# Optimization experiments

Measured on AMD Instinct MI355X. Metric: run time of the kernel, lower is better.

Reference implementation:

```python
import jax, jax.numpy as jnp
import numpy as np

B, V, E = 8, 12288, 147456
C_FM, C_U, C_IN, C_HID, C_OUT = 384, 61, 64, 128, 32
EPS = 0.005


def grid_sample_bilinear(img, grid):
    """torch.F.grid_sample, mode='bilinear', padding='zeros', align_corners=False.
    img: (B,C,H,W); grid: (B,Hg,Wg,2) in [-1,1] (x,y). Returns (B,C,Hg,Wg)."""
    Bn, C, H, W = img.shape
    x = (grid[..., 0] + 1.0) * 0.5 * W - 0.5
    y = (grid[..., 1] + 1.0) * 0.5 * H - 0.5
    x0 = jnp.floor(x); y0 = jnp.floor(y)
    wx1 = x - x0; wy1 = y - y0
    wx0 = 1.0 - wx1; wy0 = 1.0 - wy1
    x0i = x0.astype(jnp.int32); y0i = y0.astype(jnp.int32)

    def gather(iy, ix):
        valid = (ix >= 0) & (ix < W) & (iy >= 0) & (iy < H)
        ixc = jnp.clip(ix, 0, W - 1)
        iyc = jnp.clip(iy, 0, H - 1)
        v = jax.vmap(lambda im, yy, xx: im[:, yy, xx])(img, iyc, ixc)  # (B,C,Hg,Wg)
        return v * valid[:, None].astype(img.dtype)

    out = (gather(y0i, x0i) * (wy0 * wx0)[:, None]
           + gather(y0i, x0i + 1) * (wy0 * wx1)[:, None]
           + gather(y0i + 1, x0i) * (wy1 * wx0)[:, None]
           + gather(y0i + 1, x0i + 1) * (wy1 * wx1)[:, None])
    return out


def setup_inputs() -> dict:
    key = jax.random.key(0)
    ks = jax.random.split(key, 12)
    vertices = jax.random.normal(ks[0], (B, V, 3), jnp.float32) * 0.3
    fz = jnp.full((B,), 0.005, jnp.float32) + jax.random.uniform(ks[1], (B,), jnp.float32) * 0.0005
    cz = jax.random.normal(ks[2], (B, 2), jnp.float32) * 0.05
    # depth near fz*(z+100) ~ 0.5 so the |d - z| < eps visibility test fires for a subset
    depth_map = 0.5 + jax.random.normal(ks[3], (B, 1, 128, 128), jnp.float32) * 0.005
    feature_map = jax.random.normal(ks[4], (B, C_FM, 64, 64), jnp.float32)
    conv_w = jax.random.normal(ks[5], (C_U, C_FM), jnp.float32) / np.sqrt(C_FM)
    conv_b = jnp.zeros((C_U,), jnp.float32)
    W1 = jax.random.normal(ks[6], (C_IN, C_HID), jnp.float32) / np.sqrt(C_IN)
    b1 = jnp.zeros((C_HID,), jnp.float32)
    W2 = jax.random.normal(ks[7], (C_HID, C_OUT), jnp.float32) / np.sqrt(C_HID)
    W_dv = jax.random.normal(ks[8], (C_HID, 3), jnp.float32) / np.sqrt(C_HID)
    edge_row = jax.random.randint(ks[9], (E,), 0, V, jnp.int32)
    edge_col = jax.random.randint(ks[10], (E,), 0, V, jnp.int32)
    return {"feature_map": feature_map, "depth_map": depth_map, "vertices": vertices,
            "fz": fz, "cz": cz, "conv_w": conv_w, "conv_b": conv_b,
            "W1": W1, "b1": b1, "W2": W2, "W_dv": W_dv,
            "edge_row": edge_row, "edge_col": edge_col}


def reference(feature_map, depth_map, vertices, fz, cz, conv_w, conv_b,
              W1, b1, W2, W_dv, edge_row, edge_col):
    # ---- indexing(): project vertices to image plane (replicates cz[:,0] on both axes as in source) ----
    v = jnp.stack([vertices[..., 0], vertices[..., 1], vertices[..., 2] + 100.0], axis=-1)
    v = fz[:, None, None] * v
    cshift = cz[:, 0][:, None]
    v = v.at[..., 0].add(cshift).at[..., 1].add(cshift)
    grid = v[:, None, :, :2]                                     # (B,1,V,2)
    sampled_depth = grid_sample_bilinear(depth_map, grid)[:, 0, 0, :]   # (B,V)
    visible = jnp.abs(sampled_depth - v[..., 2]) < EPS           # (B,V) bool
    sf = grid_sample_bilinear(feature_map, grid)[:, :, 0, :]     # (B,C_FM,V)
    sf = sf * visible[:, None, :].astype(sf.dtype)
    # ---- 1x1 conv projection ----
    proj = jnp.einsum('oc,bcv->bov', conv_w, sf) + conv_b[None, :, None]  # (B,C_U,V)
    # ---- GCN input: concat projected features + raw vertex coords ----
    x = jnp.concatenate([proj, jnp.transpose(vertices, (0, 2, 1))], axis=1)  # (B,C_IN,V)
    x = jnp.transpose(x, (0, 2, 1))                              # (B,V,C_IN)
    # ---- sparse-adjacency message passing (row-normalized A) ----
    deg = jax.ops.segment_sum(jnp.ones((E,), x.dtype), edge_row, num_segments=V)
    deg = jnp.maximum(deg, 1.0)

    def agg(h):  # h: (B,V,C) -> A_norm @ h
        msgs = h[:, edge_col]                                    # (B,E,C) gather
        s = jax.vmap(lambda m: jax.ops.segment_sum(m, edge_row, num_segments=V))(msgs)
        return s / deg[None, :, None]

    h = jax.nn.relu(agg(x) @ W1 + b1)                            # (B,V,C_HID)
    x_out = agg(h) @ W2                                          # (B,V,C_OUT)
    dv = h @ W_dv                                                # (B,V,3)
    vertices_new = vertices + dv
    # pack (gcn features, refined verts *1000, offsets *1000) as in source scaling
    return jnp.concatenate([x_out, vertices_new * 1000.0, dv * 1000.0], axis=-1)  # (B,V,38)
```

## Files before the change

### kernel.cpp

```cpp
#include <hip/hip_runtime.h>

#define NB 8
#define NV 12288
#define NE 147456
#define CFM 384
#define CU 61
#define FEPS 0.005f

typedef unsigned short ushort_t;
typedef unsigned int uint_t;
typedef __attribute__((ext_vector_type(8))) unsigned short ushort8v;
typedef __attribute__((ext_vector_type(4))) unsigned short ushort4v;

__device__ inline float b2f(ushort_t u) {
    return __uint_as_float(((uint_t)u) << 16);
}
__device__ inline ushort_t f2b(float f) {
    uint_t u = __float_as_uint(f);
    return (ushort_t)((u + 0x7fffu + ((u >> 16) & 1u)) >> 16);
}

__global__ void k_wt(const float* __restrict__ cw, float* __restrict__ cwT) {
    int idx = blockIdx.x * 256 + threadIdx.x;
    if (idx >= CFM * 64) return;
    int c = idx >> 6, o = idx & 63;
    cwT[idx] = (o < CU) ? cw[o * CFM + c] : 0.f;
}

__global__ __launch_bounds__(512) void k_conv(const float* __restrict__ fm,
                                              const float* __restrict__ cwT,
                                              ushort_t* __restrict__ pf) {
    __shared__ float ftile[32][64];
    int tid = threadIdx.x;
    int lane = tid & 63;
    int og = __builtin_amdgcn_readfirstlane(tid >> 6);
    int idx0 = blockIdx.x * 64;
    int b = idx0 >> 12, p0 = idx0 & 4095;
    const float* fb = fm + (size_t)b * CFM * 4096 + p0;
    int sc = tid >> 4, spq = tid & 15;
    const float* saddr = fb + (size_t)sc * 4096 + spq * 4;

    float acc[8];
#pragma unroll
    for (int o = 0; o < 8; o++) acc[o] = 0.f;

    float4 nxt = *(const float4*)saddr;
    for (int cc = 0; cc < CFM; cc += 32) {
        *(float4*)&ftile[sc][spq * 4] = nxt;
        __syncthreads();
        if (cc + 32 < CFM)
            nxt = *(const float4*)(saddr + (size_t)(cc + 32) * 4096);
#pragma unroll 8
        for (int c = 0; c < 32; c++) {
            float fv = ftile[c][lane];
            const float4* w4 = (const float4*)(cwT + (cc + c) * 64 + og * 8);
            float4 wa = w4[0], wb = w4[1];
            float w[8] = {wa.x, wa.y, wa.z, wa.w, wb.x, wb.y, wb.z, wb.w};
#pragma unroll
            for (int o = 0; o < 8; o++) acc[o] = fmaf(fv, w[o], acc[o]);
        }
        __syncthreads();
    }
    uint_t pk[4];
#pragma unroll
    for (int j = 0; j < 4; j++)
        pk[j] = (uint_t)f2b(acc[2 * j]) | ((uint_t)f2b(acc[2 * j + 1]) << 16);
    uint4* outp = (uint4*)(pf + (size_t)(idx0 + lane) * 64 + og * 8);
    outp[0] = make_uint4(pk[0], pk[1], pk[2], pk[3]);
}

__global__ void k_sample(const float* __restrict__ depth, const ushort_t* __restrict__ pf,
                         const float* __restrict__ verts, const float* __restrict__ fz,
                         const float* __restrict__ cz, const float* __restrict__ convb,
                         ushort_t* __restrict__ xfeat) {
    int t = blockIdx.x * 256 + threadIdx.x;
    int gid = t >> 4;
    int ln = t & 15;
    int b = gid / NV;
    int v = gid - b * NV;
    const float* vp = verts + (size_t)gid * 3;
    float vx = vp[0], vy = vp[1], vz = vp[2];
    float fzb = fz[b], czb = cz[2 * b];
    float gx = fzb * vx + czb;
    float gy = fzb * vy + czb;
    float gz = fzb * (vz + 100.f);

    float px = (gx + 1.f) * 64.f - 0.5f;
    float py = (gy + 1.f) * 64.f - 0.5f;
    float fx0 = floorf(px), fy0 = floorf(py);
    float wx1 = px - fx0, wy1 = py - fy0, wx0 = 1.f - wx1, wy0 = 1.f - wy1;
    int x0 = (int)fx0, y0 = (int)fy0;
    const float* dmb = depth + (size_t)b * 128 * 128;
    float d00 = 0.f, d01 = 0.f, d10 = 0.f, d11 = 0.f;
    bool X0 = (x0 >= 0 && x0 < 128), X1 = (x0 + 1 >= 0 && x0 + 1 < 128);
    bool Y0 = (y0 >= 0 && y0 < 128), Y1 = (y0 + 1 >= 0 && y0 + 1 < 128);
    int xa = min(max(x0, 0), 127), xb = min(max(x0 + 1, 0), 127);
    int ya = min(max(y0, 0), 127), yb = min(max(y0 + 1, 0), 127);
    if (Y0 && X0) d00 = dmb[ya * 128 + xa];
    if (Y0 && X1) d01 = dmb[ya * 128 + xb];
    if (Y1 && X0) d10 = dmb[yb * 128 + xa];
    if (Y1 && X1) d11 = dmb[yb * 128 + xb];
    float sd = d00 * wy0 * wx0 + d01 * wy0 * wx1 + d10 * wy1 * wx0 + d11 * wy1 * wx1;
    float vis = (fabsf(sd - gz) < FEPS) ? 1.f : 0.f;

    float qx = (gx + 1.f) * 32.f - 0.5f;
    float qy = (gy + 1.f) * 32.f - 0.5f;
    float gx0 = floorf(qx), gy0 = floorf(qy);
    float ax1 = qx - gx0, ay1 = qy - gy0, ax0 = 1.f - ax1, ay0 = 1.f - ay1;
    int cx0 = (int)gx0, cy0 = (int)gy0;
    bool FX0 = (cx0 >= 0 && cx0 < 64), FX1 = (cx0 + 1 >= 0 && cx0 + 1 < 64);
    bool FY0 = (cy0 >= 0 && cy0 < 64), FY1 = (cy0 + 1 >= 0 && cy0 + 1 < 64);
    int fxa = min(max(cx0, 0), 63), fxb = min(max(cx0 + 1, 0), 63);
    int fya = min(max(cy0, 0), 63), fyb = min(max(cy0 + 1, 0), 63);
    float m00 = (FY0 && FX0) ? ay0 * ax0 : 0.f;
    float m01 = (FY0 && FX1) ? ay0 * ax1 : 0.f;
    float m10 = (FY1 && FX0) ? ay1 * ax0 : 0.f;
    float m11 = (FY1 && FX1) ? ay1 * ax1 : 0.f;
    const ushort_t* pfb = pf + (size_t)b * 4096 * 64;
    const ushort_t* p00 = pfb + ((size_t)fya * 64 + fxa) * 64;
    const ushort_t* p01 = pfb + ((size_t)fya * 64 + fxb) * 64;
    const ushort_t* p10 = pfb + ((size_t)fyb * 64 + fxa) * 64;
    const ushort_t* p11 = pfb + ((size_t)fyb * 64 + fxb) * 64;

    ushort_t* xr = xfeat + ((size_t)v * NB + b) * 64;
#pragma unroll
    for (int j = 0; j < 4; j++) {
        int c = ln + 16 * j;
        if (c < CU) {
            float val = m00 * b2f(p00[c]) + m01 * b2f(p01[c])
                      + m10 * b2f(p10[c]) + m11 * b2f(p11[c]);
            xr[c] = f2b(vis * val + convb[c]);
        } else {
            xr[c] = f2b(vp[c - CU]);
        }
    }
}

__global__ void k_count(const int* __restrict__ erow, int* __restrict__ counts) {
    int e = blockIdx.x * 256 + threadIdx.x;
    if (e < NE) atomicAdd(&counts[erow[e]], 1);
}

__global__ void k_scan(const int* __restrict__ counts, int* __restrict__ offs) {
    __shared__ int part[1024];
    int t = threadIdx.x;
    int base = t * 12;
    int local[12];
    int s = 0;
#pragma unroll
    for (int i = 0; i < 12; i++) { local[i] = s; s += counts[base + i]; }
    part[t] = s;
    __syncthreads();
    for (int off = 1; off < 1024; off <<= 1) {
        int v = (t >= off) ? part[t - off] : 0;
        __syncthreads();
        part[t] += v;
        __syncthreads();
    }
    int prefix = part[t] - s;
#pragma unroll
    for (int i = 0; i < 12; i++) offs[base + i] = prefix + local[i];
}

__global__ void k_fill(const int* __restrict__ erow, const int* __restrict__ ecol,
                       const int* __restrict__ offs, int* __restrict__ cursor,
                       int* __restrict__ csr) {
    int e = blockIdx.x * 256 + threadIdx.x;
    if (e >= NE) return;
    int r = erow[e];
    int pos = offs[r] + atomicAdd(&cursor[r], 1);
    csr[pos] = ecol[e];
}

__global__ __launch_bounds__(256) void k_gmlp(
        const int* __restrict__ counts, const int* __restrict__ offs,
        const int* __restrict__ csr, const ushort_t* __restrict__ xfeat,
        const float* __restrict__ W1, const float* __restrict__ b1,
        const float* __restrict__ W2, const float* __restrict__ Wdv,
        const float* __restrict__ verts, ushort_t* __restrict__ y2,
        float* __restrict__ out) {
    __shared__ float smem[2 * 64 * 37];
    float* xl = smem;
    float* part2 = smem;
    int tid = threadIdx.x;
    int lane = tid & 63;
    int w = __builtin_amdgcn_readfirstlane(tid >> 6);
    int vbase = blockIdx.x * 8;

#pragma unroll
    for (int s = 0; s < 2; s++) {
        int vid = vbase + 2 * w + s;
        int beg = offs[vid], n = counts[vid];
        float a[8];
#pragma unroll
        for (int t = 0; t < 8; t++) a[t] = 0.f;
        for (int j = 0; j < n; j++) {
            int c = csr[beg + j];
            ushort8v u = *(const ushort8v*)(xfeat + (size_t)c * 512 + lane * 8);
#pragma unroll
            for (int t = 0; t < 8; t++) a[t] += b2f(u[t]);
        }
        float dinv = 1.f / fmaxf((float)n, 1.f);
        float* dst = xl + ((2 * w + s) * 8 + (lane >> 3)) * 65 + (lane & 7) * 8;
#pragma unroll
        for (int t = 0; t < 8; t++) dst[t] = a[t] * dinv;
    }
    __syncthreads();

    float h[32];
    {
        const float* bp = b1 + w * 32;
#pragma unroll
        for (int j = 0; j < 32; j++) h[j] = bp[j];
    }
    const float* xrow = xl + lane * 65;
#pragma unroll 8
    for (int k = 0; k < 64; k++) {
        float xv = xrow[k];
        const float* wk = W1 + k * 128 + w * 32;
#pragma unroll
        for (int j = 0; j < 32; j++) h[j] = fmaf(xv, wk[j], h[j]);
    }
#pragma unroll
    for (int j = 0; j < 32; j++) h[j] = fmaxf(h[j], 0.f);

    float acc2[35];
#pragma unroll
    for (int j = 0; j < 35; j++) acc2[j] = 0.f;
    const float* w2p = W2 + (size_t)(w * 32) * 32;
    const float* wdp = Wdv + (size_t)(w * 32) * 3;
#pragma unroll 4
    for (int kc = 0; kc < 32; kc++) {
        float hv = h[kc];
#pragma unroll
        for (int j = 0; j < 32; j++)
            acc2[j] = fmaf(hv, w2p[kc * 32 + j], acc2[j]);
        acc2[32] = fmaf(hv, wdp[kc * 3 + 0], acc2[32]);
        acc2[33] = fmaf(hv, wdp[kc * 3 + 1], acc2[33]);
        acc2[34] = fmaf(hv, wdp[kc * 3 + 2], acc2[34]);
    }
    __syncthreads();

    if (w >= 2) {
        float* pp = part2 + ((size_t)(w - 2) * 64 + lane) * 37;
#pragma unroll
        for (int j = 0; j < 35; j++) pp[j] = acc2[j];
    }
    __syncthreads();
    if (w < 2) {
        const float* pp = part2 + ((size_t)w * 64 + lane) * 37;
#pragma unroll
        for (int j = 0; j < 35; j++) acc2[j] += pp[j];
    }
    __syncthreads();
    if (w == 1) {
        float* pp = part2 + (size_t)lane * 37;
#pragma unroll
        for (int j = 0; j < 35; j++) pp[j] = acc2[j];
    }
    __syncthreads();
    if (w == 0) {
        const float* pp = part2 + (size_t)lane * 37;
#pragma unroll
        for (int j = 0; j < 35; j++) acc2[j] += pp[j];
        int row = vbase * 8 + lane;
        uint_t pk[16];
#pragma unroll
        for (int j = 0; j < 16; j++)
            pk[j] = (uint_t)f2b(acc2[2 * j]) | ((uint_t)f2b(acc2[2 * j + 1]) << 16);
        uint4* yp = (uint4*)(y2 + (size_t)row * 32);
#pragma unroll
        for (int j = 0; j < 4; j++)
            yp[j] = make_uint4(pk[4 * j], pk[4 * j + 1], pk[4 * j + 2], pk[4 * j + 3]);
        float e0 = acc2[32], e1 = acc2[33], e2 = acc2[34];
        int v = row >> 3, b = row & 7;
        const float* vp = verts + ((size_t)b * NV + v) * 3;
        float* orow = out + ((size_t)b * NV + v) * 38;
        orow[32] = (vp[0] + e0) * 1000.f;
        orow[33] = (vp[1] + e1) * 1000.f;
        orow[34] = (vp[2] + e2) * 1000.f;
        orow[35] = e0 * 1000.f;
        orow[36] = e1 * 1000.f;
        orow[37] = e2 * 1000.f;
    }
}

__global__ void k_agg2(const int* __restrict__ counts, const int* __restrict__ offs,
                       const int* __restrict__ csr, const ushort_t* __restrict__ y2,
                       float* __restrict__ out) {
    int wid = (blockIdx.x * 256 + threadIdx.x) >> 6;
    int l = threadIdx.x & 63;
    if (wid >= NV) return;
    int beg = offs[wid], n = counts[wid];
    float a[4];
#pragma unroll
    for (int t = 0; t < 4; t++) a[t] = 0.f;
    for (int j = 0; j < n; j++) {
        int c = csr[beg + j];
        ushort4v u = *(const ushort4v*)(y2 + (size_t)c * 256 + l * 4);
#pragma unroll
        for (int t = 0; t < 4; t++) a[t] += b2f(u[t]);
    }
    float dinv = 1.f / fmaxf((float)n, 1.f);
    int b = l >> 3, o = (l & 7) * 4;
    float* orow = out + ((size_t)b * NV + wid) * 38 + o;
    orow[0] = a[0] * dinv;
    orow[1] = a[1] * dinv;
    orow[2] = a[2] * dinv;
    orow[3] = a[3] * dinv;
}

extern "C" void kernel_launch(void* const* d_in, const int* in_sizes, int n_in,
                              void* d_out, int out_size, void* d_ws, size_t ws_size,
                              hipStream_t stream) {
    const float* fm  = (const float*)d_in[0];
    const float* dm  = (const float*)d_in[1];
    const float* vt  = (const float*)d_in[2];
    const float* fz  = (const float*)d_in[3];
    const float* cz  = (const float*)d_in[4];
    const float* cw  = (const float*)d_in[5];
    const float* cb  = (const float*)d_in[6];
    const float* W1  = (const float*)d_in[7];
    const float* b1  = (const float*)d_in[8];
    const float* W2  = (const float*)d_in[9];
    const float* Wdv = (const float*)d_in[10];
    const int* erow  = (const int*)d_in[11];
    const int* ecol  = (const int*)d_in[12];
    float* out = (float*)d_out;

    float* ws    = (float*)d_ws;
    float* cwT   = ws;
    ushort_t* pf = (ushort_t*)(cwT + 24576);
    ushort_t* xfeat = (ushort_t*)((float*)pf + 1048576);
    ushort_t* y2 = (ushort_t*)((float*)xfeat + 3145728);
    int* counts  = (int*)((float*)y2 + 1572864);
    int* offs    = counts + 12288;
    int* cursor  = offs + 12288;
    int* csr     = cursor + 12288;

    hipMemsetAsync(counts, 0, 12288 * sizeof(int), stream);
    hipMemsetAsync(cursor, 0, 12288 * sizeof(int), stream);

    k_wt<<<96, 256, 0, stream>>>(cw, cwT);
    k_conv<<<512, 512, 0, stream>>>(fm, cwT, pf);
    k_sample<<<6144, 256, 0, stream>>>(dm, pf, vt, fz, cz, cb, xfeat);
    k_count<<<576, 256, 0, stream>>>(erow, counts);
    k_scan<<<1, 1024, 0, stream>>>(counts, offs);
    k_fill<<<576, 256, 0, stream>>>(erow, ecol, offs, cursor, csr);
    k_gmlp<<<1536, 256, 0, stream>>>(counts, offs, csr, xfeat,
                                     W1, b1, W2, Wdv, vt, y2, out);
    k_agg2<<<3072, 256, 0, stream>>>(counts, offs, csr, y2, out);
}
```

Baseline: 149.3 us.

## Merge independent preprocessing kernels by block-range dispatch and double-buffer conv tile

The six preprocessing launches (weight transpose, conv, sample, count, scan, fill) are packed into three kernels. Independent work is selected by block index, for example transpose with edge counting, scan with conv, and CSR fill with sampling, which removes launch gaps and lets the pieces overlap. The conv kernel now double-buffers its shared tile so one __syncthreads per iteration can be dropped. The gmlp aggregation interleaves the neighbor loops of two vertices to expose more memory-level parallelism. The scan runs in a single 512-thread block inside a launch where the other blocks do conv, so this one block could sit on the critical path.

Measured after the change: 143.8 us. -3.7%, faster.

```diff
diff --git a/kernel.cpp b/kernel.cpp
--- a/kernel.cpp
+++ b/kernel.cpp
@@ -20,21 +20,26 @@
     return (ushort_t)((u + 0x7fffu + ((u >> 16) & 1u)) >> 16);
 }
 
-__global__ void k_wt(const float* __restrict__ cw, float* __restrict__ cwT) {
-    int idx = blockIdx.x * 256 + threadIdx.x;
-    if (idx >= CFM * 64) return;
-    int c = idx >> 6, o = idx & 63;
-    cwT[idx] = (o < CU) ? cw[o * CFM + c] : 0.f;
-}
-
-__global__ __launch_bounds__(512) void k_conv(const float* __restrict__ fm,
-                                              const float* __restrict__ cwT,
-                                              ushort_t* __restrict__ pf) {
-    __shared__ float ftile[32][64];
+__global__ __launch_bounds__(512) void kL1(const float* __restrict__ cw,
+                                           float* __restrict__ cwT,
+                                           const int* __restrict__ erow,
+                                           int* __restrict__ counts) {
+    if (blockIdx.x < 48) {
+        int idx = blockIdx.x * 512 + threadIdx.x;
+        int c = idx >> 6, o = idx & 63;
+        cwT[idx] = (o < CU) ? cw[o * CFM + c] : 0.f;
+    } else {
+        int e = (blockIdx.x - 48) * 512 + threadIdx.x;
+        if (e < NE) atomicAdd(&counts[erow[e]], 1);
+    }
+}
+
+__device__ void conv_body(int bid, float* smem, const float* __restrict__ fm,
+                          const float* __restrict__ cwT, ushort_t* __restrict__ pf) {
     int tid = threadIdx.x;
     int lane = tid & 63;
     int og = __builtin_amdgcn_readfirstlane(tid >> 6);
-    int idx0 = blockIdx.x * 64;
+    int idx0 = bid * 64;
     int b = idx0 >> 12, p0 = idx0 & 4095;
     const float* fb = fm + (size_t)b * CFM * 4096 + p0;
     int sc = tid >> 4, spq = tid & 15;
@@ -45,21 +50,23 @@
     for (int o = 0; o < 8; o++) acc[o] = 0.f;
 
     float4 nxt = *(const float4*)saddr;
+    int buf = 0;
     for (int cc = 0; cc < CFM; cc += 32) {
-        *(float4*)&ftile[sc][spq * 4] = nxt;
+        float* ftb = smem + buf * 2048;
+        *(float4*)(ftb + sc * 64 + spq * 4) = nxt;
         __syncthreads();
         if (cc + 32 < CFM)
             nxt = *(const float4*)(saddr + (size_t)(cc + 32) * 4096);
 #pragma unroll 8
         for (int c = 0; c < 32; c++) {
-            float fv = ftile[c][lane];
+            float fv = ftb[c * 64 + lane];
             const float4* w4 = (const float4*)(cwT + (cc + c) * 64 + og * 8);
             float4 wa = w4[0], wb = w4[1];
             float w[8] = {wa.x, wa.y, wa.z, wa.w, wb.x, wb.y, wb.z, wb.w};
 #pragma unroll
             for (int o = 0; o < 8; o++) acc[o] = fmaf(fv, w[o], acc[o]);
         }
-        __syncthreads();
+        buf ^= 1;
     }
     uint_t pk[4];
 #pragma unroll
@@ -69,11 +76,47 @@
     outp[0] = make_uint4(pk[0], pk[1], pk[2], pk[3]);
 }
 
-__global__ void k_sample(const float* __restrict__ depth, const ushort_t* __restrict__ pf,
-                         const float* __restrict__ verts, const float* __restrict__ fz,
-                         const float* __restrict__ cz, const float* __restrict__ convb,
-                         ushort_t* __restrict__ xfeat) {
-    int t = blockIdx.x * 256 + threadIdx.x;
+__device__ void scan_body(int* ipart, const int* __restrict__ counts,
+                          int* __restrict__ offs) {
+    int t = threadIdx.x;
+    int base = t * 24;
+    int local[24];
+    int s = 0;
+#pragma unroll
+    for (int i = 0; i < 24; i++) { local[i] = s; s += counts[base + i]; }
+    ipart[t] = s;
+    __syncthreads();
+    for (int off = 1; off < 512; off <<= 1) {
+        int v = (t >= off) ? ipart[t - off] : 0;
+        __syncthreads();
+        ipart[t] += v;
+        __syncthreads();
+    }
+    int prefix = ipart[t] - s;
+#pragma unroll
+    for (int i = 0; i < 24; i++) offs[base + i] = prefix + local[i];
+}
+
+__global__ __launch_bounds__(512) void kL2(const float* __restrict__ fm,
+                                           const float* __restrict__ cwT,
+                                           ushort_t* __restrict__ pf,
+                                           const int* __restrict__ counts,
+                                           int* __restrict__ offs) {
+    __shared__ float smem[2 * 32 * 64];
+    if (blockIdx.x == 0) {
+        scan_body((int*)smem, counts, offs);
+    } else {
+        conv_body(blockIdx.x - 1, smem, fm, cwT, pf);
+    }
+}
+
+__device__ void sample_body(int t, const float* __restrict__ depth,
+                            const ushort_t* __restrict__ pf,
+                            const float* __restrict__ verts,
+                            const float* __restrict__ fz,
+                            const float* __restrict__ cz,
+                            const float* __restrict__ convb,
+                            ushort_t* __restrict__ xfeat) {
     int gid = t >> 4;
     int ln = t & 15;
     int b = gid / NV;
@@ -107,11 +150,11 @@
     float qy = (gy + 1.f) * 32.f - 0.5f;
     float gx0 = floorf(qx), gy0 = floorf(qy);
     float ax1 = qx - gx0, ay1 = qy - gy0, ax0 = 1.f - ax1, ay0 = 1.f - ay1;
-    int cx0 = (int)gx0, cy0 = (int)gy0;
-    bool FX0 = (cx0 >= 0 && cx0 < 64), FX1 = (cx0 + 1 >= 0 && cx0 + 1 < 64);
-    bool FY0 = (cy0 >= 0 && cy0 < 64), FY1 = (cy0 + 1 >= 0 && cy0 + 1 < 64);
-    int fxa = min(max(cx0, 0), 63), fxb = min(max(cx0 + 1, 0), 63);
-    int fya = min(max(cy0, 0), 63), fyb = min(max(cy0 + 1, 0), 63);
+    int icx0 = (int)gx0, icy0 = (int)gy0;
+    bool FX0 = (icx0 >= 0 && icx0 < 64), FX1 = (icx0 + 1 >= 0 && icx0 + 1 < 64);
+    bool FY0 = (icy0 >= 0 && icy0 < 64), FY1 = (icy0 + 1 >= 0 && icy0 + 1 < 64);
+    int fxa = min(max(icx0, 0), 63), fxb = min(max(icx0 + 1, 0), 63);
+    int fya = min(max(icy0, 0), 63), fyb = min(max(icy0 + 1, 0), 63);
     float m00 = (FY0 && FX0) ? ay0 * ax0 : 0.f;
     float m01 = (FY0 && FX1) ? ay0 * ax1 : 0.f;
     float m10 = (FY1 && FX0) ? ay1 * ax0 : 0.f;
@@ -136,40 +179,29 @@
     }
 }
 
-__global__ void k_count(const int* __restrict__ erow, int* __restrict__ counts) {
-    int e = blockIdx.x * 256 + threadIdx.x;
-    if (e < NE) atomicAdd(&counts[erow[e]], 1);
-}
-
-__global__ void k_scan(const int* __restrict__ counts, int* __restrict__ offs) {
-    __shared__ int part[1024];
-    int t = threadIdx.x;
-    int base = t * 12;
-    int local[12];
-    int s = 0;
-#pragma unroll
-    for (int i = 0; i < 12; i++) { local[i] = s; s += counts[base + i]; }
-    part[t] = s;
-    __syncthreads();
-    for (int off = 1; off < 1024; off <<= 1) {
-        int v = (t >= off) ? part[t - off] : 0;
-        __syncthreads();
-        part[t] += v;
-        __syncthreads();
-    }
-    int prefix = part[t] - s;
-#pragma unroll
-    for (int i = 0; i < 12; i++) offs[base + i] = prefix + local[i];
-}
-
-__global__ void k_fill(const int* __restrict__ erow, const int* __restrict__ ecol,
-                       const int* __restrict__ offs, int* __restrict__ cursor,
-                       int* __restrict__ csr) {
-    int e = blockIdx.x * 256 + threadIdx.x;
-    if (e >= NE) return;
-    int r = erow[e];
-    int pos = offs[r] + atomicAdd(&cursor[r], 1);
-    csr[pos] = ecol[e];
+__global__ __launch_bounds__(512) void kL3(const int* __restrict__ erow,
+                                           const int* __restrict__ ecol,
+                                           const int* __restrict__ offs,
+                                           int* __restrict__ cursor,
+                                           int* __restrict__ csr,
+                                           const float* __restrict__ depth,
+                                           const ushort_t* __restrict__ pf,
+                                           const float* __restrict__ verts,
+                                           const float* __restrict__ fz,
+                                           const float* __restrict__ cz,
+                                           const float* __restrict__ convb,
+                                           ushort_t* __restrict__ xfeat) {
+    if (blockIdx.x < 288) {
+        int e = blockIdx.x * 512 + threadIdx.x;
+        if (e < NE) {
+            int r = erow[e];
+            int pos = offs[r] + atomicAdd(&cursor[r], 1);
+            csr[pos] = ecol[e];
+        }
+    } else {
+        int t = (blockIdx.x - 288) * 512 + threadIdx.x;
+        sample_body(t, depth, pf, verts, fz, cz, convb, xfeat);
+    }
 }
 
 __global__ __launch_bounds__(256) void k_gmlp(
@@ -187,23 +219,36 @@
     int w = __builtin_amdgcn_readfirstlane(tid >> 6);
     int vbase = blockIdx.x * 8;
 
-#pragma unroll
-    for (int s = 0; s < 2; s++) {
-        int vid = vbase + 2 * w + s;
-        int beg = offs[vid], n = counts[vid];
-        float a[8];
-#pragma unroll
-        for (int t = 0; t < 8; t++) a[t] = 0.f;
-        for (int j = 0; j < n; j++) {
-            int c = csr[beg + j];
-            ushort8v u = *(const ushort8v*)(xfeat + (size_t)c * 512 + lane * 8);
-#pragma unroll
-            for (int t = 0; t < 8; t++) a[t] += b2f(u[t]);
+    {
+        int vid = vbase + 2 * w;
+        int beg0 = offs[vid], n0 = counts[vid];
+        int beg1 = offs[vid + 1], n1 = counts[vid + 1];
+        float a0[8], a1[8];
+#pragma unroll
+        for (int t = 0; t < 8; t++) { a0[t] = 0.f; a1[t] = 0.f; }
+        int nmax = max(n0, n1);
+        for (int j = 0; j < nmax; j++) {
+            if (j < n0) {
+                int c = csr[beg0 + j];
+                ushort8v u = *(const ushort8v*)(xfeat + (size_t)c * 512 + lane * 8);
+#pragma unroll
+                for (int t = 0; t < 8; t++) a0[t] += b2f(u[t]);
+            }
+            if (j < n1) {
+                int c = csr[beg1 + j];
+                ushort8v u = *(const ushort8v*)(xfeat + (size_t)c * 512 + lane * 8);
+#pragma unroll
+                for (int t = 0; t < 8; t++) a1[t] += b2f(u[t]);
+            }
         }
-        float dinv = 1.f / fmaxf((float)n, 1.f);
-        float* dst = xl + ((2 * w + s) * 8 + (lane >> 3)) * 65 + (lane & 7) * 8;
-#pragma unroll
-        for (int t = 0; t < 8; t++) dst[t] = a[t] * dinv;
+        float d0 = 1.f / fmaxf((float)n0, 1.f);
+        float d1 = 1.f / fmaxf((float)n1, 1.f);
+        float* dst0 = xl + ((2 * w) * 8 + (lane >> 3)) * 65 + (lane & 7) * 8;
+        float* dst1 = xl + ((2 * w + 1) * 8 + (lane >> 3)) * 65 + (lane & 7) * 8;
+#pragma unroll
+        for (int t = 0; t < 8; t++) dst0[t] = a0[t] * d0;
+#pragma unroll
+        for (int t = 0; t < 8; t++) dst1[t] = a1[t] * d1;
     }
     __syncthreads();
 
@@ -341,12 +386,10 @@
     hipMemsetAsync(counts, 0, 12288 * sizeof(int), stream);
     hipMemsetAsync(cursor, 0, 12288 * sizeof(int), stream);
 
-    k_wt<<<96, 256, 0, stream>>>(cw, cwT);
-    k_conv<<<512, 512, 0, stream>>>(fm, cwT, pf);
-    k_sample<<<6144, 256, 0, stream>>>(dm, pf, vt, fz, cz, cb, xfeat);
-    k_count<<<576, 256, 0, stream>>>(erow, counts);
-    k_scan<<<1, 1024, 0, stream>>>(counts, offs);
-    k_fill<<<576, 256, 0, stream>>>(erow, ecol, offs, cursor, csr);
+    kL1<<<336, 512, 0, stream>>>(cw, cwT, erow, counts);
+    kL2<<<513, 512, 0, stream>>>(fm, cwT, pf, counts, offs);
+    kL3<<<3360, 512, 0, stream>>>(erow, ecol, offs, cursor, csr,
+                                  dm, pf, vt, fz, cz, cb, xfeat);
     k_gmlp<<<1536, 256, 0, stream>>>(counts, offs, csr, xfeat,
                                      W1, b1, W2, Wdv, vt, y2, out);
     k_agg2<<<3072, 256, 0, stream>>>(counts, offs, csr, y2, out);
```
